# Optimization experiments

Measured on AMD Instinct MI355X. Metric: run time of the kernel, lower is better.

The kernel has to match this reference:

```python
import jax, jax.numpy as jnp
import numpy as np

H = 16
D_MODEL = 1024
HEAD = D_MODEL // H  # 64
B, S = 2, 2048
NEG = -1e9


def setup_inputs() -> dict:
    key = jax.random.key(0)
    ks = jax.random.split(key, 12)
    sd = 1.0 / np.sqrt(D_MODEL)
    inp = {
        "query": jax.random.normal(ks[0], (B, S, D_MODEL), jnp.float32),
        "key": jax.random.normal(ks[1], (B, S, D_MODEL), jnp.float32),
        "value": jax.random.normal(ks[2], (B, S, D_MODEL), jnp.float32),
        "mask": jax.random.randint(ks[3], (B, 1, S, S), 0, 2, jnp.int32),
        "Wq": jax.random.normal(ks[4], (D_MODEL, H * HEAD), jnp.float32) * sd,
        "bq": jnp.zeros((H * HEAD,), jnp.float32),
        "Wk": jax.random.normal(ks[5], (D_MODEL, H * HEAD), jnp.float32) * sd,
        "bk": jnp.zeros((H * HEAD,), jnp.float32),
        "Wv": jax.random.normal(ks[6], (D_MODEL, H * HEAD), jnp.float32) * sd,
        "bv": jnp.zeros((H * HEAD,), jnp.float32),
        "Wo": jax.random.normal(ks[7], (H * HEAD, D_MODEL), jnp.float32) * sd,
        "bo": jnp.zeros((D_MODEL,), jnp.float32),
    }
    return inp


def reference(query, key, value, mask, Wq, bq, Wk, bk, Wv, bv, Wo, bo):
    b = query.shape[0]
    # project and split heads: [b, s, h*d] -> [b, h, s, d]
    def split_heads(x):
        return x.reshape(b, -1, H, HEAD).transpose(0, 2, 1, 3)
    q = split_heads(query @ Wq + bq)
    k = split_heads(key @ Wk + bk)
    v = split_heads(value @ Wv + bv)
    scores = jnp.einsum("bhqd,bhkd->bhqk", q, k) / jnp.sqrt(jnp.float32(HEAD))
    scores = jnp.where(mask == 0, NEG, scores)
    p_attn = jax.nn.softmax(scores, axis=-1)  # dropout: eval mode (identity)
    x = jnp.einsum("bhqk,bhkd->bhqd", p_attn, v)
    x = x.transpose(0, 2, 1, 3).reshape(b, -1, H * HEAD)
    return x @ Wo + bo
```

## Files before the change

kernel.cpp:

```cpp
#include <hip/hip_runtime.h>
#include <hip/hip_bf16.h>

#define H 16
#define S 2048
#define DM 1024
#define HD 64
#define NB 2
#define LOG2E 1.4426950408889634f

typedef __attribute__((ext_vector_type(8))) short short8_t;
typedef __attribute__((ext_vector_type(4))) float f32x4;
typedef __attribute__((ext_vector_type(16))) float f32x16;

static __device__ __forceinline__ unsigned short f2bf(float f){
  union { float f; unsigned u; } x; x.f = f;
  unsigned r = x.u + 0x7fffu + ((x.u >> 16) & 1u);
  return (unsigned short)(r >> 16);
}

static __device__ __forceinline__ unsigned pk2(float a, float b){
  union { __hip_bfloat16 h; unsigned short u; } x, y;
  x.h = __hip_bfloat16(a); y.h = __hip_bfloat16(b);
  return (unsigned)x.u | ((unsigned)y.u << 16);
}

static __device__ __forceinline__ float ex2(float x){
#if __has_builtin(__builtin_amdgcn_exp2f)
  return __builtin_amdgcn_exp2f(x);
#else
  return exp2f(x);
#endif
}

static __device__ __forceinline__ void pswap(unsigned &x, unsigned &y){
#if defined(__gfx950__) || defined(__AMDGCN__)
  asm("v_permlane32_swap_b32 %0, %1" : "+v"(x), "+v"(y));
#else
  unsigned sx = (unsigned)__shfl_xor((int)x, 32);
  unsigned sy = (unsigned)__shfl_xor((int)y, 32);
  bool hi = (threadIdx.x & 63) >= 32;
  unsigned nx = hi ? sy : x;
  unsigned ny = hi ? y : sx;
  x = nx; y = ny;
#endif
}

__global__ __launch_bounds__(256) void prep(const float* __restrict__ q, const float* __restrict__ k,
    const float* __restrict__ v, const int* __restrict__ mask,
    const float* __restrict__ Wq, const float* __restrict__ Wk, const float* __restrict__ Wv,
    const float* __restrict__ Wo,
    unsigned short* __restrict__ qb, unsigned short* __restrict__ kb, unsigned short* __restrict__ vb,
    unsigned short* __restrict__ WT, unsigned short* __restrict__ WoT,
    unsigned short* __restrict__ m16){
  __shared__ float tt[32][33];
  const int bid = blockIdx.x, tid = threadIdx.x;
  if (bid < 6144){
    const int w = bid >> 11;
    const int blk = bid & 2047;
    const float* src = (w==0)? q : (w==1)? k : v;
    unsigned short* dst = (w==0)? qb : (w==1)? kb : vb;
    size_t i = ((size_t)blk*256 + tid)*8;
    float4 x = *(const float4*)(src + i);
    float4 y = *(const float4*)(src + i + 4);
    ushort4 o1{f2bf(x.x),f2bf(x.y),f2bf(x.z),f2bf(x.w)};
    ushort4 o2{f2bf(y.x),f2bf(y.y),f2bf(y.z),f2bf(y.w)};
    *(ushort4*)(dst+i) = o1; *(ushort4*)(dst+i+4) = o2;
  } else if (bid < 8192){
    size_t base = ((size_t)(bid-6144)*256 + tid)*16;
    unsigned u = 0;
    #pragma unroll
    for (int j2=0;j2<4;j2++){
      int4 mm = *(const int4*)(mask + base + j2*4);
      u |= (mm.x!=0 ? 1u:0u) << (j2*4);
      u |= (mm.y!=0 ? 1u:0u) << (j2*4+1);
      u |= (mm.z!=0 ? 1u:0u) << (j2*4+2);
      u |= (mm.w!=0 ? 1u:0u) << (j2*4+3);
    }
    m16[base>>4] = (unsigned short)u;
  } else {
    const int wb = bid - 8192;
    const int widx = wb >> 10, t = wb & 1023;
    const float* W = (widx==0)? Wq : (widx==1)? Wk : (widx==2)? Wv : Wo;
    unsigned short* dst = (widx<3)? (WT + (size_t)widx*DM*DM) : WoT;
    const int tx = tid & 31, ty = tid >> 5;
    const int r0 = (t >> 5) * 32, c0 = (t & 31) * 32;
    #pragma unroll
    for (int i2=0;i2<32;i2+=8) tt[ty+i2][tx] = W[(size_t)(r0+ty+i2)*DM + c0+tx];
    __syncthreads();
    #pragma unroll
    for (int i2=0;i2<32;i2+=8) dst[(size_t)(c0+ty+i2)*DM + r0+tx] = f2bf(tt[tx][ty+i2]);
  }
}

__global__ __launch_bounds__(256, 2) void qkv_gemm(
    const unsigned short* __restrict__ qb, const unsigned short* __restrict__ kb,
    const unsigned short* __restrict__ vb2, const unsigned short* __restrict__ WT,
    const float* __restrict__ bq, const float* __restrict__ bk, const float* __restrict__ bv,
    unsigned short* __restrict__ Qp, unsigned short* __restrict__ Kp, unsigned short* __restrict__ VTp){
  __shared__ __align__(16) char Al[2][8192];
  __shared__ __align__(16) char Bl[2][8192];
  const int tid = threadIdx.x, lane = tid & 63, wv = tid >> 6;
  const int l15 = lane & 15, l4 = lane >> 4;
  const int wr = wv >> 1, wc = wv & 1;
  const int p = blockIdx.x >> 3;
  const int n0 = (blockIdx.x & 7) * 128;
  const int m0 = blockIdx.y * 128;
  const unsigned short* A = (p==0)? qb : (p==1)? kb : vb2;
  const unsigned short* Bt = WT + (size_t)blockIdx.x * 128 * DM;
  const float* bias = (p==0)? bq : (p==1)? bk : bv;

  f32x4 acc[4][4];
  #pragma unroll
  for (int i=0;i<4;i++)
    #pragma unroll
    for (int j=0;j<4;j++) acc[i][j] = (f32x4){0.f,0.f,0.f,0.f};

  const char* ga[2]; const char* gb[2];
  #pragma unroll
  for (int i=0;i<2;i++){
    int u = tid + i*256, c = u>>6, l = u&63;
    ga[i] = (const char*)A  + ((size_t)(m0 + c*16 + (l&15))*DM + (l>>4)*8)*2;
    gb[i] = (const char*)Bt + ((size_t)(c*16 + (l&15))*DM + (l>>4)*8)*2;
  }
  const int lo0 = tid*16, lo1 = tid*16 + 4096;

  uint4 ra0 = *(const uint4*)ga[0], ra1 = *(const uint4*)ga[1];
  uint4 rb0 = *(const uint4*)gb[0], rb1 = *(const uint4*)gb[1];
  *(uint4*)(Al[0]+lo0)=ra0; *(uint4*)(Al[0]+lo1)=ra1;
  *(uint4*)(Bl[0]+lo0)=rb0; *(uint4*)(Bl[0]+lo1)=rb1;
  __syncthreads();

  const bool sw = (p==2);
  const int NT = DM/32;
  int pb = 0;
  for (int t=0;t<NT;t++){
    if (t+1 < NT){
      ra0 = *(const uint4*)(ga[0] + (size_t)(t+1)*64);
      ra1 = *(const uint4*)(ga[1] + (size_t)(t+1)*64);
      rb0 = *(const uint4*)(gb[0] + (size_t)(t+1)*64);
      rb1 = *(const uint4*)(gb[1] + (size_t)(t+1)*64);
    }
    short8_t av[4], bvv[4];
    #pragma unroll
    for (int i=0;i<4;i++) av[i]  = *(const short8_t*)(Al[pb] + (wr*4+i)*1024 + lane*16);
    #pragma unroll
    for (int j=0;j<4;j++) bvv[j] = *(const short8_t*)(Bl[pb] + (wc*4+j)*1024 + lane*16);
    __builtin_amdgcn_s_setprio(1);
    if (sw){
      #pragma unroll
      for (int i=0;i<4;i++)
        #pragma unroll
        for (int j=0;j<4;j++)
          acc[i][j] = __builtin_amdgcn_mfma_f32_16x16x32_bf16(bvv[j], av[i], acc[i][j], 0,0,0);
    } else {
      #pragma unroll
      for (int i=0;i<4;i++)
        #pragma unroll
        for (int j=0;j<4;j++)
          acc[i][j] = __builtin_amdgcn_mfma_f32_16x16x32_bf16(av[i], bvv[j], acc[i][j], 0,0,0);
    }
    __builtin_amdgcn_s_setprio(0);
    if (t+1 < NT){
      *(uint4*)(Al[pb^1]+lo0)=ra0; *(uint4*)(Al[pb^1]+lo1)=ra1;
      *(uint4*)(Bl[pb^1]+lo0)=rb0; *(uint4*)(Bl[pb^1]+lo1)=rb1;
    }
    __syncthreads();
    pb ^= 1;
  }

  if (!sw){
    unsigned short* out = (p==0)? Qp : Kp;
    const float scl = (p==0)? 0.125f*LOG2E : 1.0f;
    #pragma unroll
    for (int i=0;i<4;i++)
      #pragma unroll
      for (int j=0;j<4;j++)
        #pragma unroll
        for (int jr=0;jr<4;jr++){
          int m = m0 + wr*64 + i*16 + l4*4 + jr;
          int n = n0 + wc*64 + j*16 + l15;
          float val = (acc[i][j][jr] + bias[n]) * scl;
          int b2 = m >> 11, s = m & (S-1), hh2 = n >> 6, d = n & 63;
          out[(((size_t)b2*H + hh2)*S + s)*HD + d] = f2bf(val);
        }
  } else {
    #pragma unroll
    for (int i=0;i<4;i++)
      #pragma unroll
      for (int j=0;j<4;j++)
        #pragma unroll
        for (int jr=0;jr<4;jr++){
          int n = n0 + wc*64 + j*16 + l4*4 + jr;
          int m = m0 + wr*64 + i*16 + l15;
          float val = acc[i][j][jr] + bias[n];
          int b2 = m >> 11, s = m & (S-1), hh2 = n >> 6, d = n & 63;
          VTp[(((size_t)b2*H + hh2)*HD + d)*S + s] = f2bf(val);
        }
  }
}

__global__ __launch_bounds__(256, 2) void out_gemm(const unsigned short* __restrict__ A,
    const unsigned short* __restrict__ WoT, const float* __restrict__ bo, float* __restrict__ out){
  __shared__ __align__(16) char Al[2][8192];
  __shared__ __align__(16) char Bl[2][4096];
  const int tid = threadIdx.x, lane = tid & 63, wv = tid >> 6;
  const int l15 = lane & 15, l4 = lane >> 4;
  const int wr = wv >> 1, wc = wv & 1;
  const int n0 = blockIdx.x * 64;
  const int m0 = blockIdx.y * 128;

  f32x4 acc[4][2];
  #pragma unroll
  for (int i=0;i<4;i++)
    #pragma unroll
    for (int j=0;j<2;j++) acc[i][j] = (f32x4){0.f,0.f,0.f,0.f};

  const char* ga[2]; const char* gbp;
  #pragma unroll
  for (int i=0;i<2;i++){
    int u = tid + i*256, c = u>>6, l = u&63;
    ga[i] = (const char*)A + ((size_t)(m0 + c*16 + (l&15))*DM + (l>>4)*8)*2;
  }
  {
    int c = tid>>6, l = tid&63;
    gbp = (const char*)WoT + ((size_t)(n0 + c*16 + (l&15))*DM + (l>>4)*8)*2;
  }
  const int lo0 = tid*16, lo1 = tid*16 + 4096;

  uint4 ra0 = *(const uint4*)ga[0], ra1 = *(const uint4*)ga[1], rb0 = *(const uint4*)gbp;
  *(uint4*)(Al[0]+lo0)=ra0; *(uint4*)(Al[0]+lo1)=ra1; *(uint4*)(Bl[0]+lo0)=rb0;
  __syncthreads();

  const int NT = DM/32;
  int pb = 0;
  for (int t=0;t<NT;t++){
    if (t+1 < NT){
      ra0 = *(const uint4*)(ga[0] + (size_t)(t+1)*64);
      ra1 = *(const uint4*)(ga[1] + (size_t)(t+1)*64);
      rb0 = *(const uint4*)(gbp  + (size_t)(t+1)*64);
    }
    short8_t av[4], bvv[2];
    #pragma unroll
    for (int i=0;i<4;i++) av[i]  = *(const short8_t*)(Al[pb] + (wr*4+i)*1024 + lane*16);
    #pragma unroll
    for (int j=0;j<2;j++) bvv[j] = *(const short8_t*)(Bl[pb] + (wc*2+j)*1024 + lane*16);
    __builtin_amdgcn_s_setprio(1);
    #pragma unroll
    for (int i=0;i<4;i++)
      #pragma unroll
      for (int j=0;j<2;j++)
        acc[i][j] = __builtin_amdgcn_mfma_f32_16x16x32_bf16(av[i], bvv[j], acc[i][j], 0,0,0);
    __builtin_amdgcn_s_setprio(0);
    if (t+1 < NT){
      *(uint4*)(Al[pb^1]+lo0)=ra0; *(uint4*)(Al[pb^1]+lo1)=ra1; *(uint4*)(Bl[pb^1]+lo0)=rb0;
    }
    __syncthreads();
    pb ^= 1;
  }

  #pragma unroll
  for (int i=0;i<4;i++)
    #pragma unroll
    for (int j=0;j<2;j++)
      #pragma unroll
      for (int jr=0;jr<4;jr++){
        int m = m0 + wr*64 + i*16 + l4*4 + jr;
        int n = n0 + wc*32 + j*16 + l15;
        out[(size_t)m*DM + n] = acc[i][j][jr] + bo[n];
      }
}

__global__ __launch_bounds__(256, 2) void attn_fwd(const unsigned short* __restrict__ Qp,
    const unsigned short* __restrict__ Kp, const unsigned short* __restrict__ VTp,
    const unsigned long long* __restrict__ Mb, unsigned short* __restrict__ X){
  __shared__ __align__(16) char smem[32768];
  const int tid = threadIdx.x, lane = tid & 63, wv = tid >> 6;
  const int q31 = lane & 31, h = lane >> 5;
  const int bh = blockIdx.y, b = bh >> 4, hh = bh & 15;
  const int q0 = blockIdx.x * 128;
  const int qrow = q0 + wv*32 + q31;

  const unsigned short* Qb = Qp + ((size_t)bh*S + qrow)*HD;
  short8_t qf[4];
  #pragma unroll
  for (int ks=0;ks<4;ks++) qf[ks] = *(const short8_t*)(Qb + ks*16 + h*8);

  short8_t ones8;
  #pragma unroll
  for (int j2=0;j2<8;j2++) ones8[j2] = (short)0x3F80;

  f32x16 o0, o1, aS;
  #pragma unroll
  for (int r=0;r<16;r++){ o0[r]=0.f; o1[r]=0.f; aS[r]=0.f; }
  float mrun = -3.0e38f;

  const char* KsrcB = (const char*)(Kp + (size_t)bh*S*HD);
  const char* VsrcB = (const char*)(VTp + (size_t)bh*HD*S);
  const unsigned long long* mrow = Mb + ((size_t)b*S + qrow)*(S/64);

  const char* kg[2]; const char* vg[2]; int ldso[2];
  #pragma unroll
  for (int i=0;i<2;i++){
    int u = tid + i*256, c = u>>6, l = u&63;
    kg[i] = KsrcB + ((size_t)(32*(c>>2) + (l&31))*HD + (c&3)*16 + (l>>5)*8)*2;
    vg[i] = VsrcB + ((size_t)(32*(c>>2) + (l&31))*S  + (c&3)*16 + (l>>5)*8)*2;
    ldso[i] = u*16;
  }

  uint4 kr0 = *(const uint4*)kg[0], kr1 = *(const uint4*)kg[1];
  uint4 vr0 = *(const uint4*)vg[0], vr1 = *(const uint4*)vg[1];
  unsigned long long wnx = mrow[0];
  *(uint4*)(smem + ldso[0]) = kr0; *(uint4*)(smem + ldso[1]) = kr1;
  *(uint4*)(smem + 16384 + ldso[0]) = vr0; *(uint4*)(smem + 16384 + ldso[1]) = vr1;
  __syncthreads();

  const int NT = S/64;
  int pb = 0;
  for (int t=0; t<NT; ++t){
    unsigned long long wcur = wnx;
    if (t+1 < NT){
      kr0 = *(const uint4*)(kg[0] + (size_t)(t+1)*8192);
      kr1 = *(const uint4*)(kg[1] + (size_t)(t+1)*8192);
      vr0 = *(const uint4*)(vg[0] + (size_t)(t+1)*128);
      vr1 = *(const uint4*)(vg[1] + (size_t)(t+1)*128);
      wnx = mrow[t+1];
    }
    const char* kb = smem + pb*8192;
    const char* vb = smem + 16384 + pb*8192;

    f32x16 c0, c1;
    #pragma unroll
    for (int r=0;r<16;r++){ c0[r]=0.f; c1[r]=0.f; }
    __builtin_amdgcn_s_setprio(1);
    #pragma unroll
    for (int ks=0;ks<4;ks++){
      short8_t kf0 = *(const short8_t*)(kb + ks*1024 + lane*16);
      c0 = __builtin_amdgcn_mfma_f32_32x32x16_bf16(kf0, qf[ks], c0, 0,0,0);
      short8_t kf1 = *(const short8_t*)(kb + (4+ks)*1024 + lane*16);
      c1 = __builtin_amdgcn_mfma_f32_32x32x16_bf16(kf1, qf[ks], c1, 0,0,0);
    }
    __builtin_amdgcn_s_setprio(0);

    float mf = c0[0];
    #pragma unroll
    for (int r=1;r<16;r++) mf = fmaxf(mf, c0[r]);
    #pragma unroll
    for (int r=0;r<16;r++) mf = fmaxf(mf, c1[r]);
    mf = fmaxf(mf, __shfl_xor(mf, 32));
    if (!__all(mf <= mrun + 8.0f)){
      float mnew = fmaxf(mrun, mf);
      float rs = ex2(mrun - mnew);
      mrun = mnew;
      #pragma unroll
      for (int r=0;r<16;r++){ o0[r]*=rs; o1[r]*=rs; }
      aS[0]*=rs;
    }

    unsigned long long wsh = wcur >> (4*h);
    unsigned mlo = (unsigned)wsh, mhi = (unsigned)(wsh >> 32);
    #pragma unroll
    for (int r=0;r<16;r++){
      const int bitc = (r&3) + 8*(r>>2);
      float e0 = ex2(c0[r] - mrun);
      float e1 = ex2(c1[r] - mrun);
      c0[r] = ((mlo >> bitc) & 1u) ? e0 : 0.f;
      c1[r] = ((mhi >> bitc) & 1u) ? e1 : 0.f;
    }

    unsigned w0[8], w1[8];
    #pragma unroll
    for (int m=0;m<8;m++){ w0[m] = pk2(c0[2*m], c0[2*m+1]); w1[m] = pk2(c1[2*m], c1[2*m+1]); }
    union Frag { short8_t s; unsigned w[4]; };
    Frag pf[4];
    { unsigned x=w0[0], y=w0[2]; pswap(x,y); pf[0].w[0]=x; pf[0].w[2]=y; }
    { unsigned x=w0[1], y=w0[3]; pswap(x,y); pf[0].w[1]=x; pf[0].w[3]=y; }
    { unsigned x=w0[4], y=w0[6]; pswap(x,y); pf[1].w[0]=x; pf[1].w[2]=y; }
    { unsigned x=w0[5], y=w0[7]; pswap(x,y); pf[1].w[1]=x; pf[1].w[3]=y; }
    { unsigned x=w1[0], y=w1[2]; pswap(x,y); pf[2].w[0]=x; pf[2].w[2]=y; }
    { unsigned x=w1[1], y=w1[3]; pswap(x,y); pf[2].w[1]=x; pf[2].w[3]=y; }
    { unsigned x=w1[4], y=w1[6]; pswap(x,y); pf[3].w[0]=x; pf[3].w[2]=y; }
    { unsigned x=w1[5], y=w1[7]; pswap(x,y); pf[3].w[1]=x; pf[3].w[3]=y; }

    __builtin_amdgcn_s_setprio(1);
    #pragma unroll
    for (int kvs=0;kvs<4;kvs++){
      aS = __builtin_amdgcn_mfma_f32_32x32x16_bf16(ones8, pf[kvs].s, aS, 0,0,0);
      short8_t vf0 = *(const short8_t*)(vb + kvs*1024 + lane*16);
      o0 = __builtin_amdgcn_mfma_f32_32x32x16_bf16(vf0, pf[kvs].s, o0, 0,0,0);
      short8_t vf1 = *(const short8_t*)(vb + (4+kvs)*1024 + lane*16);
      o1 = __builtin_amdgcn_mfma_f32_32x32x16_bf16(vf1, pf[kvs].s, o1, 0,0,0);
    }
    __builtin_amdgcn_s_setprio(0);

    if (t+1 < NT){
      char* kw = smem + (pb^1)*8192;
      char* vw = smem + 16384 + (pb^1)*8192;
      *(uint4*)(kw + ldso[0]) = kr0; *(uint4*)(kw + ldso[1]) = kr1;
      *(uint4*)(vw + ldso[0]) = vr0; *(uint4*)(vw + ldso[1]) = vr1;
    }
    __syncthreads();
    pb ^= 1;
  }

  float inv = 1.0f / aS[0];
  const int ql = wv*32 + q31;
  #pragma unroll
  for (int m=0;m<8;m++){
    int d0 = ((2*m)&3) + 8*(m>>1) + 4*h;
    unsigned wa = pk2(o0[2*m]*inv, o0[2*m+1]*inv);
    *(unsigned*)(smem + ql*128 + (((d0>>3) ^ (ql&7))*16) + (d0&7)*2) = wa;
    int d1 = d0 + 32;
    unsigned wb2 = pk2(o1[2*m]*inv, o1[2*m+1]*inv);
    *(unsigned*)(smem + ql*128 + (((d1>>3) ^ (ql&7))*16) + (d1&7)*2) = wb2;
  }
  __syncthreads();
  #pragma unroll
  for (int it=0; it<4; it++){
    int u = it*256 + tid;
    int row = u>>3, cc = u&7;
    uint4 vvv = *(const uint4*)(smem + row*128 + cc*16);
    int g = cc ^ (row & 7);
    *(uint4*)(X + ((size_t)b*S + q0 + row)*DM + hh*HD + g*8) = vvv;
  }
}

extern "C" void kernel_launch(void* const* d_in, const int* in_sizes, int n_in,
                              void* d_out, int out_size, void* d_ws, size_t ws_size,
                              hipStream_t stream){
  const float* query = (const float*)d_in[0];
  const float* key   = (const float*)d_in[1];
  const float* value = (const float*)d_in[2];
  const int*   mask  = (const int*)d_in[3];
  const float* Wq = (const float*)d_in[4];
  const float* bq = (const float*)d_in[5];
  const float* Wk = (const float*)d_in[6];
  const float* bk = (const float*)d_in[7];
  const float* Wv = (const float*)d_in[8];
  const float* bvp= (const float*)d_in[9];
  const float* Wo = (const float*)d_in[10];
  const float* bo = (const float*)d_in[11];

  const size_t NE = (size_t)NB*S*DM;
  const size_t WE = (size_t)DM*DM;
  const size_t ME = (size_t)NB*S*S;

  char* w = (char*)d_ws;
  unsigned short* qb  = (unsigned short*)w; w += NE*2;
  unsigned short* kb  = (unsigned short*)w; w += NE*2;
  unsigned short* vb  = (unsigned short*)w; w += NE*2;
  unsigned short* WT  = (unsigned short*)w; w += 3*WE*2;
  unsigned short* WoT = (unsigned short*)w; w += WE*2;
  unsigned short* m16 = (unsigned short*)w; w += (ME/16)*2;
  unsigned short* Qp  = (unsigned short*)w; w += NE*2;
  unsigned short* Kp  = (unsigned short*)w; w += NE*2;
  unsigned short* VTp = (unsigned short*)w; w += NE*2;
  unsigned short* xb  = (unsigned short*)w; w += NE*2;

  prep<<<12288, 256, 0, stream>>>(query, key, value, mask, Wq, Wk, Wv, Wo,
                                  qb, kb, vb, WT, WoT, m16);
  qkv_gemm<<<dim3(24,32), 256, 0, stream>>>(qb, kb, vb, WT, bq, bk, bvp, Qp, Kp, VTp);
  attn_fwd<<<dim3(S/128, NB*H), 256, 0, stream>>>(Qp, Kp, VTp,
                                  (const unsigned long long*)m16, xb);
  out_gemm<<<dim3(DM/64, (NB*S)/128), 256, 0, stream>>>(xb, WoT, bo, (float*)d_out);
}
```

Baseline: 300.7 us.

## Use direct global-to-LDS async loads in GEMMs and attention; transpose mask bits

Replaces the register-staged global→LDS tile copies in qkv_gemm, out_gemm and attn_fwd with global_load_lds direct-to-LDS transfers, freeing VGPRs and removing the explicit ds_write step. The mask bitmap is rewritten in prep into a column-block-major layout so attention can stage a contiguous 64-row mask chunk into LDS per tile. The launch_bounds occupancy hint of 2 is also dropped. The risk is that synchronisation relies only on __syncthreads around async LDS writes, with no explicit vmcnt wait, and the __syncthreads sits after the prefetch for the next tile is issued.

```diff
diff --git a/kernel.cpp b/kernel.cpp
--- a/kernel.cpp
+++ b/kernel.cpp
@@ -30,6 +30,12 @@
 #else
   return exp2f(x);
 #endif
+}
+
+static __device__ __forceinline__ void async16(void* lds, const void* g){
+  __builtin_amdgcn_global_load_lds(
+      (const __attribute__((address_space(1))) unsigned int*)g,
+      (__attribute__((address_space(3))) unsigned int*)lds, 16, 0, 0);
 }
 
 static __device__ __forceinline__ void pswap(unsigned &x, unsigned &y){
@@ -51,8 +57,9 @@
     const float* __restrict__ Wo,
     unsigned short* __restrict__ qb, unsigned short* __restrict__ kb, unsigned short* __restrict__ vb,
     unsigned short* __restrict__ WT, unsigned short* __restrict__ WoT,
-    unsigned short* __restrict__ m16){
+    unsigned long long* __restrict__ mT){
   __shared__ float tt[32][33];
+  __shared__ unsigned short ml[64][4];
   const int bid = blockIdx.x, tid = threadIdx.x;
   if (bid < 6144){
     const int w = bid >> 11;
@@ -66,17 +73,28 @@
     ushort4 o2{f2bf(y.x),f2bf(y.y),f2bf(y.z),f2bf(y.w)};
     *(ushort4*)(dst+i) = o1; *(ushort4*)(dst+i+4) = o2;
   } else if (bid < 8192){
-    size_t base = ((size_t)(bid-6144)*256 + tid)*16;
+    const int mt = bid - 6144;
+    const int b2 = mt >> 10, rb = (mt >> 5) & 31, cb = mt & 31;
+    const int r = tid >> 2, cq = tid & 3;
+    const int* src = mask + ((size_t)b2*S + rb*64 + r)*S + cb*64 + cq*16;
     unsigned u = 0;
     #pragma unroll
     for (int j2=0;j2<4;j2++){
-      int4 mm = *(const int4*)(mask + base + j2*4);
+      int4 mm = *(const int4*)(src + j2*4);
       u |= (mm.x!=0 ? 1u:0u) << (j2*4);
       u |= (mm.y!=0 ? 1u:0u) << (j2*4+1);
       u |= (mm.z!=0 ? 1u:0u) << (j2*4+2);
       u |= (mm.w!=0 ? 1u:0u) << (j2*4+3);
     }
-    m16[base>>4] = (unsigned short)u;
+    ml[r][cq] = (unsigned short)u;
+    __syncthreads();
+    if (tid < 64){
+      unsigned long long w64 = (unsigned long long)ml[tid][0]
+        | ((unsigned long long)ml[tid][1] << 16)
+        | ((unsigned long long)ml[tid][2] << 32)
+        | ((unsigned long long)ml[tid][3] << 48);
+      mT[((size_t)b2*32 + cb)*S + rb*64 + tid] = w64;
+    }
   } else {
     const int wb = bid - 8192;
     const int widx = wb >> 10, t = wb & 1023;
@@ -92,7 +110,7 @@
   }
 }
 
-__global__ __launch_bounds__(256, 2) void qkv_gemm(
+__global__ __launch_bounds__(256) void qkv_gemm(
     const unsigned short* __restrict__ qb, const unsigned short* __restrict__ kb,
     const unsigned short* __restrict__ vb2, const unsigned short* __restrict__ WT,
     const float* __restrict__ bq, const float* __restrict__ bk, const float* __restrict__ bv,
@@ -115,31 +133,33 @@
     #pragma unroll
     for (int j=0;j<4;j++) acc[i][j] = (f32x4){0.f,0.f,0.f,0.f};
 
-  const char* ga[2]; const char* gb[2];
-  #pragma unroll
-  for (int i=0;i<2;i++){
-    int u = tid + i*256, c = u>>6, l = u&63;
-    ga[i] = (const char*)A  + ((size_t)(m0 + c*16 + (l&15))*DM + (l>>4)*8)*2;
-    gb[i] = (const char*)Bt + ((size_t)(c*16 + (l&15))*DM + (l>>4)*8)*2;
-  }
-  const int lo0 = tid*16, lo1 = tid*16 + 4096;
-
-  uint4 ra0 = *(const uint4*)ga[0], ra1 = *(const uint4*)ga[1];
-  uint4 rb0 = *(const uint4*)gb[0], rb1 = *(const uint4*)gb[1];
-  *(uint4*)(Al[0]+lo0)=ra0; *(uint4*)(Al[0]+lo1)=ra1;
-  *(uint4*)(Bl[0]+lo0)=rb0; *(uint4*)(Bl[0]+lo1)=rb1;
+  const char *ga0, *ga1, *gb0, *gb1;
+  {
+    int u = tid, c = u>>6, l = u&63;
+    ga0 = (const char*)A  + ((size_t)(m0 + c*16 + (l&15))*DM + (l>>4)*8)*2;
+    gb0 = (const char*)Bt + ((size_t)(c*16 + (l&15))*DM + (l>>4)*8)*2;
+    u = tid + 256; c = u>>6; l = u&63;
+    ga1 = (const char*)A  + ((size_t)(m0 + c*16 + (l&15))*DM + (l>>4)*8)*2;
+    gb1 = (const char*)Bt + ((size_t)(c*16 + (l&15))*DM + (l>>4)*8)*2;
+  }
+  const int wb16 = wv*1024;
+
+  auto stage = [&](int buf, int t){
+    size_t o = (size_t)t*64;
+    async16(&Al[buf][wb16],        ga0 + o);
+    async16(&Al[buf][4096+wb16],   ga1 + o);
+    async16(&Bl[buf][wb16],        gb0 + o);
+    async16(&Bl[buf][4096+wb16],   gb1 + o);
+  };
+
+  stage(0, 0);
   __syncthreads();
 
   const bool sw = (p==2);
   const int NT = DM/32;
   int pb = 0;
   for (int t=0;t<NT;t++){
-    if (t+1 < NT){
-      ra0 = *(const uint4*)(ga[0] + (size_t)(t+1)*64);
-      ra1 = *(const uint4*)(ga[1] + (size_t)(t+1)*64);
-      rb0 = *(const uint4*)(gb[0] + (size_t)(t+1)*64);
-      rb1 = *(const uint4*)(gb[1] + (size_t)(t+1)*64);
-    }
+    if (t+1 < NT) stage(pb^1, t+1);
     short8_t av[4], bvv[4];
     #pragma unroll
     for (int i=0;i<4;i++) av[i]  = *(const short8_t*)(Al[pb] + (wr*4+i)*1024 + lane*16);
@@ -160,10 +180,6 @@
           acc[i][j] = __builtin_amdgcn_mfma_f32_16x16x32_bf16(av[i], bvv[j], acc[i][j], 0,0,0);
     }
     __builtin_amdgcn_s_setprio(0);
-    if (t+1 < NT){
-      *(uint4*)(Al[pb^1]+lo0)=ra0; *(uint4*)(Al[pb^1]+lo1)=ra1;
-      *(uint4*)(Bl[pb^1]+lo0)=rb0; *(uint4*)(Bl[pb^1]+lo1)=rb1;
-    }
     __syncthreads();
     pb ^= 1;
   }
@@ -199,7 +215,7 @@
   }
 }
 
-__global__ __launch_bounds__(256, 2) void out_gemm(const unsigned short* __restrict__ A,
+__global__ __launch_bounds__(256) void out_gemm(const unsigned short* __restrict__ A,
     const unsigned short* __restrict__ WoT, const float* __restrict__ bo, float* __restrict__ out){
   __shared__ __align__(16) char Al[2][8192];
   __shared__ __align__(16) char Bl[2][4096];
@@ -215,30 +231,30 @@
     #pragma unroll
     for (int j=0;j<2;j++) acc[i][j] = (f32x4){0.f,0.f,0.f,0.f};
 
-  const char* ga[2]; const char* gbp;
-  #pragma unroll
-  for (int i=0;i<2;i++){
-    int u = tid + i*256, c = u>>6, l = u&63;
-    ga[i] = (const char*)A + ((size_t)(m0 + c*16 + (l&15))*DM + (l>>4)*8)*2;
-  }
+  const char *ga0, *ga1, *gbp;
   {
-    int c = tid>>6, l = tid&63;
+    int u = tid, c = u>>6, l = u&63;
+    ga0 = (const char*)A + ((size_t)(m0 + c*16 + (l&15))*DM + (l>>4)*8)*2;
     gbp = (const char*)WoT + ((size_t)(n0 + c*16 + (l&15))*DM + (l>>4)*8)*2;
-  }
-  const int lo0 = tid*16, lo1 = tid*16 + 4096;
-
-  uint4 ra0 = *(const uint4*)ga[0], ra1 = *(const uint4*)ga[1], rb0 = *(const uint4*)gbp;
-  *(uint4*)(Al[0]+lo0)=ra0; *(uint4*)(Al[0]+lo1)=ra1; *(uint4*)(Bl[0]+lo0)=rb0;
+    u = tid + 256; c = u>>6; l = u&63;
+    ga1 = (const char*)A + ((size_t)(m0 + c*16 + (l&15))*DM + (l>>4)*8)*2;
+  }
+  const int wb16 = wv*1024;
+
+  auto stage = [&](int buf, int t){
+    size_t o = (size_t)t*64;
+    async16(&Al[buf][wb16],      ga0 + o);
+    async16(&Al[buf][4096+wb16], ga1 + o);
+    async16(&Bl[buf][wb16],      gbp + o);
+  };
+
+  stage(0, 0);
   __syncthreads();
 
   const int NT = DM/32;
   int pb = 0;
   for (int t=0;t<NT;t++){
-    if (t+1 < NT){
-      ra0 = *(const uint4*)(ga[0] + (size_t)(t+1)*64);
-      ra1 = *(const uint4*)(ga[1] + (size_t)(t+1)*64);
-      rb0 = *(const uint4*)(gbp  + (size_t)(t+1)*64);
-    }
+    if (t+1 < NT) stage(pb^1, t+1);
     short8_t av[4], bvv[2];
     #pragma unroll
     for (int i=0;i<4;i++) av[i]  = *(const short8_t*)(Al[pb] + (wr*4+i)*1024 + lane*16);
@@ -251,9 +267,6 @@
       for (int j=0;j<2;j++)
         acc[i][j] = __builtin_amdgcn_mfma_f32_16x16x32_bf16(av[i], bvv[j], acc[i][j], 0,0,0);
     __builtin_amdgcn_s_setprio(0);
-    if (t+1 < NT){
-      *(uint4*)(Al[pb^1]+lo0)=ra0; *(uint4*)(Al[pb^1]+lo1)=ra1; *(uint4*)(Bl[pb^1]+lo0)=rb0;
-    }
     __syncthreads();
     pb ^= 1;
   }
@@ -270,10 +283,10 @@
       }
 }
 
-__global__ __launch_bounds__(256, 2) void attn_fwd(const unsigned short* __restrict__ Qp,
+__global__ __launch_bounds__(256) void attn_fwd(const unsigned short* __restrict__ Qp,
     const unsigned short* __restrict__ Kp, const unsigned short* __restrict__ VTp,
-    const unsigned long long* __restrict__ Mb, unsigned short* __restrict__ X){
-  __shared__ __align__(16) char smem[32768];
+    const unsigned long long* __restrict__ mT, unsigned short* __restrict__ X){
+  __shared__ __align__(16) char sm[34816];
   const int tid = threadIdx.x, lane = tid & 63, wv = tid >> 6;
   const int q31 = lane & 31, h = lane >> 5;
   const int bh = blockIdx.y, b = bh >> 4, hh = bh & 15;
@@ -296,37 +309,38 @@
 
   const char* KsrcB = (const char*)(Kp + (size_t)bh*S*HD);
   const char* VsrcB = (const char*)(VTp + (size_t)bh*HD*S);
-  const unsigned long long* mrow = Mb + ((size_t)b*S + qrow)*(S/64);
-
-  const char* kg[2]; const char* vg[2]; int ldso[2];
-  #pragma unroll
-  for (int i=0;i<2;i++){
-    int u = tid + i*256, c = u>>6, l = u&63;
-    kg[i] = KsrcB + ((size_t)(32*(c>>2) + (l&31))*HD + (c&3)*16 + (l>>5)*8)*2;
-    vg[i] = VsrcB + ((size_t)(32*(c>>2) + (l&31))*S  + (c&3)*16 + (l>>5)*8)*2;
-    ldso[i] = u*16;
-  }
-
-  uint4 kr0 = *(const uint4*)kg[0], kr1 = *(const uint4*)kg[1];
-  uint4 vr0 = *(const uint4*)vg[0], vr1 = *(const uint4*)vg[1];
-  unsigned long long wnx = mrow[0];
-  *(uint4*)(smem + ldso[0]) = kr0; *(uint4*)(smem + ldso[1]) = kr1;
-  *(uint4*)(smem + 16384 + ldso[0]) = vr0; *(uint4*)(smem + 16384 + ldso[1]) = vr1;
+
+  const char *kg0, *kg1, *vg0, *vg1, *mg;
+  {
+    int u = tid, c = u>>6, l = u&63;
+    kg0 = KsrcB + ((size_t)(32*(c>>2) + (l&31))*HD + (c&3)*16 + (l>>5)*8)*2;
+    vg0 = VsrcB + ((size_t)(32*(c>>2) + (l&31))*S  + (c&3)*16 + (l>>5)*8)*2;
+    u = tid + 256; c = u>>6; l = u&63;
+    kg1 = KsrcB + ((size_t)(32*(c>>2) + (l&31))*HD + (c&3)*16 + (l>>5)*8)*2;
+    vg1 = VsrcB + ((size_t)(32*(c>>2) + (l&31))*S  + (c&3)*16 + (l>>5)*8)*2;
+    mg  = (const char*)(mT + ((size_t)b*32)*S + q0) + lane*16;
+  }
+  const int wb16 = wv*1024;
+
+  auto stage = [&](int buf, int t){
+    size_t ko = (size_t)t*8192, vo = (size_t)t*128;
+    async16(&sm[buf*8192 + wb16],          kg0 + ko);
+    async16(&sm[buf*8192 + 4096 + wb16],   kg1 + ko);
+    async16(&sm[16384 + buf*8192 + wb16],        vg0 + vo);
+    async16(&sm[16384 + buf*8192 + 4096 + wb16], vg1 + vo);
+    if (wv == 0) async16(&sm[32768 + buf*1024], mg + (size_t)t*16384);
+  };
+
+  stage(0, 0);
   __syncthreads();
 
   const int NT = S/64;
   int pb = 0;
   for (int t=0; t<NT; ++t){
-    unsigned long long wcur = wnx;
-    if (t+1 < NT){
-      kr0 = *(const uint4*)(kg[0] + (size_t)(t+1)*8192);
-      kr1 = *(const uint4*)(kg[1] + (size_t)(t+1)*8192);
-      vr0 = *(const uint4*)(vg[0] + (size_t)(t+1)*128);
-      vr1 = *(const uint4*)(vg[1] + (size_t)(t+1)*128);
-      wnx = mrow[t+1];
-    }
-    const char* kb = smem + pb*8192;
-    const char* vb = smem + 16384 + pb*8192;
+    if (t+1 < NT) stage(pb^1, t+1);
+    const char* kb = sm + pb*8192;
+    const char* vb = sm + 16384 + pb*8192;
+    unsigned long long wcur = *(const unsigned long long*)(sm + 32768 + pb*1024 + (wv*32+q31)*8);
 
     f32x16 c0, c1;
     #pragma unroll
@@ -392,12 +406,6 @@
     }
     __builtin_amdgcn_s_setprio(0);
 
-    if (t+1 < NT){
-      char* kw = smem + (pb^1)*8192;
-      char* vw = smem + 16384 + (pb^1)*8192;
-      *(uint4*)(kw + ldso[0]) = kr0; *(uint4*)(kw + ldso[1]) = kr1;
-      *(uint4*)(vw + ldso[0]) = vr0; *(uint4*)(vw + ldso[1]) = vr1;
-    }
     __syncthreads();
     pb ^= 1;
   }
@@ -408,17 +416,17 @@
   for (int m=0;m<8;m++){
     int d0 = ((2*m)&3) + 8*(m>>1) + 4*h;
     unsigned wa = pk2(o0[2*m]*inv, o0[2*m+1]*inv);
-    *(unsigned*)(smem + ql*128 + (((d0>>3) ^ (ql&7))*16) + (d0&7)*2) = wa;
+    *(unsigned*)(sm + ql*128 + (((d0>>3) ^ (ql&7))*16) + (d0&7)*2) = wa;
     int d1 = d0 + 32;
     unsigned wb2 = pk2(o1[2*m]*inv, o1[2*m+1]*inv);
-    *(unsigned*)(smem + ql*128 + (((d1>>3) ^ (ql&7))*16) + (d1&7)*2) = wb2;
+    *(unsigned*)(sm + ql*128 + (((d1>>3) ^ (ql&7))*16) + (d1&7)*2) = wb2;
   }
   __syncthreads();
   #pragma unroll
   for (int it=0; it<4; it++){
     int u = it*256 + tid;
     int row = u>>3, cc = u&7;
-    uint4 vvv = *(const uint4*)(smem + row*128 + cc*16);
+    uint4 vvv = *(const uint4*)(sm + row*128 + cc*16);
     int g = cc ^ (row & 7);
     *(uint4*)(X + ((size_t)b*S + q0 + row)*DM + hh*HD + g*8) = vvv;
   }
@@ -442,7 +450,6 @@
 
   const size_t NE = (size_t)NB*S*DM;
   const size_t WE = (size_t)DM*DM;
-  const size_t ME = (size_t)NB*S*S;
 
   char* w = (char*)d_ws;
   unsigned short* qb  = (unsigned short*)w; w += NE*2;
@@ -450,16 +457,15 @@
   unsigned short* vb  = (unsigned short*)w; w += NE*2;
   unsigned short* WT  = (unsigned short*)w; w += 3*WE*2;
   unsigned short* WoT = (unsigned short*)w; w += WE*2;
-  unsigned short* m16 = (unsigned short*)w; w += (ME/16)*2;
+  unsigned long long* mT = (unsigned long long*)w; w += (size_t)NB*32*S*8;
   unsigned short* Qp  = (unsigned short*)w; w += NE*2;
   unsigned short* Kp  = (unsigned short*)w; w += NE*2;
   unsigned short* VTp = (unsigned short*)w; w += NE*2;
   unsigned short* xb  = (unsigned short*)w; w += NE*2;
 
   prep<<<12288, 256, 0, stream>>>(query, key, value, mask, Wq, Wk, Wv, Wo,
-                                  qb, kb, vb, WT, WoT, m16);
+                                  qb, kb, vb, WT, WoT, mT);
   qkv_gemm<<<dim3(24,32), 256, 0, stream>>>(qb, kb, vb, WT, bq, bk, bvp, Qp, Kp, VTp);
-  attn_fwd<<<dim3(S/128, NB*H), 256, 0, stream>>>(Qp, Kp, VTp,
-                                  (const unsigned long long*)m16, xb);
+  attn_fwd<<<dim3(S/128, NB*H), 256, 0, stream>>>(Qp, Kp, VTp, mT, xb);
   out_gemm<<<dim3(DM/64, (NB*S)/128), 256, 0, stream>>>(xb, WoT, bo, (float*)d_out);
 }
```

After: 335.5 us. 1.12x slower.
